# Performance work log

Measured on AMD Instinct MI355X. Metric: run time of the kernel, lower is better.

Reference implementation:

```python
import jax, jax.numpy as jnp
import numpy as np

B, N = 8, 48
NEMBED, EMBED_DIM, HID_DIM = 1000, 32, 32
IN_DIM = EMBED_DIM + 1  # feature dim after concatenating xfeat
N_OPS = 8  # exchangeable 3-tensor basis: identity + means over each nonempty axis subset


def setup_inputs() -> dict:
    key = jax.random.key(0)
    k1, k2, k3, k4, k5 = jax.random.split(key, 5)
    xcat = jax.random.randint(k1, (B, N), 0, NEMBED)
    xfeat = jax.random.normal(k2, (B, N), dtype=jnp.float32)
    embed_table = jax.random.normal(k3, (NEMBED, EMBED_DIM), dtype=jnp.float32)
    # SetEq3to3 coefficients: (in_dim, n_basis_ops, out_dim), Glorot-ish scale
    coefs = jax.random.normal(k4, (IN_DIM, N_OPS, HID_DIM), dtype=jnp.float32) * np.sqrt(2.0 / (IN_DIM + HID_DIM))
    eq_bias = jnp.zeros((HID_DIM,), dtype=jnp.float32)
    out_w = jax.random.normal(k5, (HID_DIM, 1), dtype=jnp.float32) * np.sqrt(1.0 / HID_DIM)
    out_b = jnp.zeros((1,), dtype=jnp.float32)
    return {"xcat": xcat, "xfeat": xfeat, "embed_table": embed_table,
            "coefs": coefs, "eq_bias": eq_bias, "out_w": out_w, "out_b": out_b}


def _set_eq3to3(t, coefs, eq_bias):
    # t: (B, d, n, n, n); coefs: (d, 8, h). Each basis op is a mean over a
    # subset of the three set axes (kept as size-1 dims so broadcasting restores shape).
    def mix(op, s):
        return jnp.einsum('bd...,dh->bh...', op, coefs[:, s, :])
    m_i = t.mean(axis=2, keepdims=True)
    m_j = t.mean(axis=3, keepdims=True)
    m_k = t.mean(axis=4, keepdims=True)
    m_ij = m_i.mean(axis=3, keepdims=True)
    m_ik = m_i.mean(axis=4, keepdims=True)
    m_jk = m_j.mean(axis=4, keepdims=True)
    m_ijk = m_ij.mean(axis=4, keepdims=True)
    out = (mix(t, 0) + mix(m_i, 1) + mix(m_j, 2) + mix(m_k, 3)
           + mix(m_ij, 4) + mix(m_ik, 5) + mix(m_jk, 6) + mix(m_ijk, 7))
    return out + eq_bias.reshape(1, -1, 1, 1, 1)  # (B, h, n, n, n)


def reference(xcat, xfeat, embed_table, coefs, eq_bias, out_w, out_b):
    e = embed_table[xcat]                                   # (B, n, d_e)
    x = jnp.concatenate([e, xfeat[..., None]], axis=-1)      # (B, n, d) with d = d_e + 1
    t = jnp.einsum('bid,bjd,bkd->bdijk', x, x, x)            # (B, d, n, n, n)
    y = _set_eq3to3(t, coefs, eq_bias)                       # (B, h, n, n, n)
    y = jnp.transpose(y, (0, 2, 3, 4, 1))                    # (B, n, n, n, h)
    y = jax.nn.relu(y)
    y = y.mean(axis=(1, 2, 3))                               # (B, h) mean pool
    y = jax.nn.relu(y)
    # dropout is inactive in eval mode (training=False)
    return y @ out_w + out_b                                 # (B, 1)
```

## Files before the change

kernel.cpp:

```cpp
#include <hip/hip_runtime.h>
#include <cstdint>
#include <cstddef>

#define BB 8
#define NN 48
#define DD 33
#define XS 40
#define KP 128
#define HH 32
#define MM (NN*NN)
#define NC (NN*HH)
#define TILE 96
#define TM (MM/TILE)
#define TN (NC/TILE)
#define NBLK (TM*TN)
#define LDK 136
#define ABLK (BB*MM/16)
#define BBLK (BB*NC/16)

typedef __attribute__((ext_vector_type(8))) _Float16 f16x8;
typedef __attribute__((ext_vector_type(4))) float f32x4;

__global__ void k_setup(const int* __restrict__ xcat, const float* __restrict__ xfeat,
                        const float* __restrict__ embed, const float* __restrict__ coefs,
                        const float* __restrict__ eq_bias,
                        float* __restrict__ xw, float* __restrict__ sw,
                        float* __restrict__ ct, float* __restrict__ gk) {
    int b = blockIdx.x, t = threadIdx.x;
    __shared__ float sl[XS];
    if (b < BB) {
        for (int idx = t; idx < NN * XS; idx += 256) {
            int i = idx / XS, d = idx - i * XS;
            float v = 0.f;
            if (d < 32)       v = embed[xcat[b * NN + i] * 32 + d];
            else if (d == 32) v = xfeat[b * NN + i];
            xw[b * NN * XS + idx] = v;
        }
        __syncthreads();
        if (t < XS) {
            float a = 0.f;
            for (int i = 0; i < NN; ++i) a += xw[b * NN * XS + i * XS + t];
            float s = a * (1.0f / 48.0f);
            sw[b * XS + t] = s;
            sl[t] = s;
        }
        __syncthreads();
        for (int idx = t; idx < NC; idx += 256) {
            int k = idx >> 5, h = idx & 31;
            const float* xk = xw + (b * NN + k) * XS;
            float g = 0.f;
            for (int d = 0; d < DD; ++d) {
                float sd = sl[d];
                g += sd * sd * (coefs[(d * 8 + 4) * HH + h] * xk[d]
                              + coefs[(d * 8 + 7) * HH + h] * sd);
            }
            gk[b * NC + idx] = g + eq_bias[h];
        }
    } else {
        for (int idx = t; idx < 8 * HH * XS; idx += 256) {
            int qh = idx / XS, d = idx - qh * XS;
            int q = qh >> 5, h = qh & 31;
            ct[idx] = (d < DD) ? coefs[(d * 8 + q) * HH + h] : 0.f;
        }
    }
}

__global__ __launch_bounds__(256) void k_build(
        const float* __restrict__ xw, const float* __restrict__ sw,
        const float* __restrict__ ct, const float* __restrict__ gk,
        _Float16* __restrict__ Aw, _Float16* __restrict__ Bw) {
    int t = threadIdx.x, blk = blockIdx.x;
    if (blk < ABLK) {
        int g = blk * 256 + t;
        int row = g >> 4, d0 = (g & 15) * 8;
        int b = row / MM, grow = row - b * MM;
        int i = grow / NN, j = grow - i * NN;
        const float* xb = xw + b * NN * XS;
        const float* sb = sw + b * XS;
        f16x8 v;
        if (d0 < 120) {
            int seg = (d0 >= 80) ? 2 : (d0 >= 40) ? 1 : 0;
            int d = d0 - seg * 40;
            const float* p1 = (seg == 2) ? (xb + j * XS) : (xb + i * XS);
            const float* p2 = (seg == 0) ? (xb + j * XS) : sb;
            f32x4 a0 = *(const f32x4*)(p1 + d), a1 = *(const f32x4*)(p1 + d + 4);
            f32x4 b0 = *(const f32x4*)(p2 + d), b1 = *(const f32x4*)(p2 + d + 4);
            f32x4 r0 = a0 * b0, r1 = a1 * b1;
            for (int e = 0; e < 4; ++e) { v[e] = (_Float16)r0[e]; v[4 + e] = (_Float16)r1[e]; }
        } else {
            v = (f16x8){0, 0, 0, 0, 0, 0, 0, 0};
            v[0] = (_Float16)1.f;
        }
        *(f16x8*)&Aw[(size_t)row * KP + d0] = v;
    } else {
        int g = (blk - ABLK) * 256 + t;
        int row = g >> 4, d0 = (g & 15) * 8;
        int b = row / NC, n = row - b * NC;
        int k = n >> 5, h = n & 31;
        const float* xk = xw + (b * NN + k) * XS;
        const float* sb = sw + b * XS;
        f16x8 v;
        if (d0 < 120) {
            int seg = (d0 >= 80) ? 2 : (d0 >= 40) ? 1 : 0;
            int d = d0 - seg * 40;
            const int QA[3] = {0, 2, 1}, QB[3] = {3, 6, 5};
            const float* ca = ct + (QA[seg] * HH + h) * XS + d;
            const float* cb = ct + (QB[seg] * HH + h) * XS + d;
            f32x4 ca0 = *(const f32x4*)(ca),     ca1 = *(const f32x4*)(ca + 4);
            f32x4 cb0 = *(const f32x4*)(cb),     cb1 = *(const f32x4*)(cb + 4);
            f32x4 xk0 = *(const f32x4*)(xk + d), xk1 = *(const f32x4*)(xk + d + 4);
            f32x4 sb0 = *(const f32x4*)(sb + d), sb1 = *(const f32x4*)(sb + d + 4);
            f32x4 r0 = ca0 * xk0 + cb0 * sb0;
            f32x4 r1 = ca1 * xk1 + cb1 * sb1;
            for (int e = 0; e < 4; ++e) { v[e] = (_Float16)r0[e]; v[4 + e] = (_Float16)r1[e]; }
        } else {
            v = (f16x8){0, 0, 0, 0, 0, 0, 0, 0};
            v[0] = (_Float16)gk[b * NC + n];
        }
        *(f16x8*)&Bw[(size_t)row * KP + d0] = v;
    }
}

__global__ __launch_bounds__(256, 3) void k_gemm(
        const _Float16* __restrict__ Aw, const _Float16* __restrict__ Bw,
        float* __restrict__ partials) {
    __shared__ __align__(16) _Float16 As[TILE][LDK];
    __shared__ __align__(16) _Float16 Bs[TILE][LDK];
    __shared__ float hacc[HH];

    int t = threadIdx.x;
    int bx = blockIdx.x, by = blockIdx.y, b = blockIdx.z;
    int N0 = bx * TILE, M0 = by * TILE;
    const _Float16* Ag = Aw + ((size_t)(b * MM + M0)) * KP;
    const _Float16* Bg = Bw + ((size_t)(b * NC + N0)) * KP;

    if (t < HH) hacc[t] = 0.f;

#pragma unroll
    for (int c = 0; c < 6; ++c) {
        int ch = c * 256 + t;
        int row = ch >> 4, d0 = (ch & 15) * 8;
        f16x8 va = *(const f16x8*)(Ag + row * KP + d0);
        f16x8 vb = *(const f16x8*)(Bg + row * KP + d0);
        *(f16x8*)&As[row][d0] = va;
        *(f16x8*)&Bs[row][d0] = vb;
    }
    __syncthreads();

    int lane = t & 63, wave = t >> 6;
    int wm = (wave >> 1) * 48, wn = (wave & 1) * 48;
    int lrow = lane & 15, quad = lane >> 4;

    f32x4 acc[3][3];
#pragma unroll
    for (int m3 = 0; m3 < 3; ++m3)
#pragma unroll
        for (int nt = 0; nt < 3; ++nt)
            acc[m3][nt] = (f32x4){0.f, 0.f, 0.f, 0.f};

#pragma unroll
    for (int ks = 0; ks < 4; ++ks) {
        f16x8 af[3], bf[3];
#pragma unroll
        for (int m3 = 0; m3 < 3; ++m3)
            af[m3] = *(const f16x8*)&As[wm + m3 * 16 + lrow][ks * 32 + quad * 8];
#pragma unroll
        for (int nt = 0; nt < 3; ++nt)
            bf[nt] = *(const f16x8*)&Bs[wn + nt * 16 + lrow][ks * 32 + quad * 8];
#pragma unroll
        for (int m3 = 0; m3 < 3; ++m3)
#pragma unroll
            for (int nt = 0; nt < 3; ++nt)
                acc[m3][nt] = __builtin_amdgcn_mfma_f32_16x16x32_f16(af[m3], bf[nt], acc[m3][nt], 0, 0, 0);
    }

    float fs[3] = {0.f, 0.f, 0.f};
#pragma unroll
    for (int m3 = 0; m3 < 3; ++m3)
#pragma unroll
        for (int nt = 0; nt < 3; ++nt)
#pragma unroll
            for (int r = 0; r < 4; ++r)
                fs[nt] += fmaxf(acc[m3][nt][r], 0.f);

#pragma unroll
    for (int nt = 0; nt < 3; ++nt) {
        float v = fs[nt];
        v += __shfl_xor(v, 16);
        v += __shfl_xor(v, 32);
        if (lane < 16) atomicAdd(&hacc[(wn + nt * 16 + lane) & 31], v);
    }
    __syncthreads();
    if (t < HH) {
        int blockLin = by * TN + bx;
        partials[((size_t)b * NBLK + blockLin) * HH + t] = hacc[t];
    }
}

__global__ void k_final(const float* __restrict__ partials, const float* __restrict__ out_w,
                        const float* __restrict__ out_b, float* __restrict__ out) {
    __shared__ float red[256];
    int b = blockIdx.x, t = threadIdx.x;
    int h = t & 31, g = t >> 5;
    float a = 0.f;
    for (int p = g; p < NBLK; p += 8) a += partials[((size_t)b * NBLK + p) * HH + h];
    red[t] = a;
    __syncthreads();
    if (t < HH) {
        float tot = 0.f;
        for (int gg = 0; gg < 8; ++gg) tot += red[gg * 32 + t];
        float m = tot * (1.0f / 110592.0f);
        red[t] = fmaxf(m, 0.f) * out_w[t];
    }
    __syncthreads();
    if (t == 0) {
        float o = 0.f;
        for (int h2 = 0; h2 < HH; ++h2) o += red[h2];
        out[b] = o + out_b[0];
    }
}

extern "C" void kernel_launch(void* const* d_in, const int* in_sizes, int n_in,
                              void* d_out, int out_size, void* d_ws, size_t ws_size,
                              hipStream_t stream) {
    (void)in_sizes; (void)n_in; (void)out_size; (void)ws_size;
    const int*   xcat    = (const int*)d_in[0];
    const float* xfeat   = (const float*)d_in[1];
    const float* embed   = (const float*)d_in[2];
    const float* coefs   = (const float*)d_in[3];
    const float* eq_bias = (const float*)d_in[4];
    const float* out_w   = (const float*)d_in[5];
    const float* out_b   = (const float*)d_in[6];
    float* out = (float*)d_out;

    char* w = (char*)d_ws;
    float*    xw       = (float*)(w + 0);
    float*    sw       = (float*)(w + 61440);
    float*    ct       = (float*)(w + 62720);
    float*    gk       = (float*)(w + 103680);
    _Float16* Aw       = (_Float16*)(w + 152832);
    _Float16* Bw       = (_Float16*)(w + 4871424);
    float*    partials = (float*)(w + 8017152);

    k_setup<<<dim3(BB + 1), dim3(256), 0, stream>>>(xcat, xfeat, embed, coefs, eq_bias,
                                                    xw, sw, ct, gk);
    k_build<<<dim3(ABLK + BBLK), dim3(256), 0, stream>>>(xw, sw, ct, gk, Aw, Bw);
    k_gemm<<<dim3(TN, TM, BB), dim3(256), 0, stream>>>(Aw, Bw, partials);
    k_final<<<dim3(BB), dim3(256), 0, stream>>>(partials, out_w, out_b, out);
}
```

Measured before the change: 108.7 us.

## Use direct global-to-LDS loads with XOR swizzle in GEMM tile staging

The GEMM kernel now stages its A and B tiles with global_load_lds direct-to-LDS 16-byte loads instead of going through registers. The padded shared layout is replaced by an unpadded one with an XOR swizzle on the source addresses, so the later fragment reads avoid bank conflicts. The setup kernel also caches the embedded rows and two coefficient slices in shared memory instead of rereading global memory. This relies on the per-wave contiguous LDS destination semantics of the builtin and on matching the swizzle between the write and read sides.

```diff
diff --git a/kernel.cpp b/kernel.cpp
--- a/kernel.cpp
+++ b/kernel.cpp
@@ -14,12 +14,17 @@
 #define TM (MM/TILE)
 #define TN (NC/TILE)
 #define NBLK (TM*TN)
-#define LDK 136
 #define ABLK (BB*MM/16)
 #define BBLK (BB*NC/16)
 
 typedef __attribute__((ext_vector_type(8))) _Float16 f16x8;
 typedef __attribute__((ext_vector_type(4))) float f32x4;
+
+__device__ __forceinline__ void gload16(const void* g, void* l) {
+    __builtin_amdgcn_global_load_lds(
+        (const __attribute__((address_space(1))) unsigned int*)g,
+        (__attribute__((address_space(3))) unsigned int*)l, 16, 0, 0);
+}
 
 __global__ void k_setup(const int* __restrict__ xcat, const float* __restrict__ xfeat,
                         const float* __restrict__ embed, const float* __restrict__ coefs,
@@ -27,19 +32,27 @@
                         float* __restrict__ xw, float* __restrict__ sw,
                         float* __restrict__ ct, float* __restrict__ gk) {
     int b = blockIdx.x, t = threadIdx.x;
-    __shared__ float sl[XS];
     if (b < BB) {
+        __shared__ float xl[NN * XS];
+        __shared__ float sl[XS];
+        __shared__ float c47[2][DD][HH];
+        for (int idx = t; idx < 2 * DD * HH; idx += 256) {
+            int q = idx / (DD * HH), r = idx - q * DD * HH;
+            int d = r >> 5, h = r & 31;
+            c47[q][d][h] = coefs[(d * 8 + (q ? 7 : 4)) * HH + h];
+        }
         for (int idx = t; idx < NN * XS; idx += 256) {
             int i = idx / XS, d = idx - i * XS;
             float v = 0.f;
             if (d < 32)       v = embed[xcat[b * NN + i] * 32 + d];
             else if (d == 32) v = xfeat[b * NN + i];
+            xl[idx] = v;
             xw[b * NN * XS + idx] = v;
         }
         __syncthreads();
         if (t < XS) {
             float a = 0.f;
-            for (int i = 0; i < NN; ++i) a += xw[b * NN * XS + i * XS + t];
+            for (int i = 0; i < NN; ++i) a += xl[i * XS + t];
             float s = a * (1.0f / 48.0f);
             sw[b * XS + t] = s;
             sl[t] = s;
@@ -47,12 +60,10 @@
         __syncthreads();
         for (int idx = t; idx < NC; idx += 256) {
             int k = idx >> 5, h = idx & 31;
-            const float* xk = xw + (b * NN + k) * XS;
             float g = 0.f;
             for (int d = 0; d < DD; ++d) {
                 float sd = sl[d];
-                g += sd * sd * (coefs[(d * 8 + 4) * HH + h] * xk[d]
-                              + coefs[(d * 8 + 7) * HH + h] * sd);
+                g += sd * sd * (c47[0][d][h] * xl[k * XS + d] + c47[1][d][h] * sd);
             }
             gk[b * NC + idx] = g + eq_bias[h];
         }
@@ -124,31 +135,29 @@
 __global__ __launch_bounds__(256, 3) void k_gemm(
         const _Float16* __restrict__ Aw, const _Float16* __restrict__ Bw,
         float* __restrict__ partials) {
-    __shared__ __align__(16) _Float16 As[TILE][LDK];
-    __shared__ __align__(16) _Float16 Bs[TILE][LDK];
+    __shared__ __align__(16) _Float16 AsF[TILE * KP];
+    __shared__ __align__(16) _Float16 BsF[TILE * KP];
     __shared__ float hacc[HH];
 
     int t = threadIdx.x;
+    int lane = t & 63, wave = t >> 6;
     int bx = blockIdx.x, by = blockIdx.y, b = blockIdx.z;
     int N0 = bx * TILE, M0 = by * TILE;
-    const _Float16* Ag = Aw + ((size_t)(b * MM + M0)) * KP;
-    const _Float16* Bg = Bw + ((size_t)(b * NC + N0)) * KP;
+    const char* Agc = (const char*)(Aw + ((size_t)(b * MM + M0)) * KP);
+    const char* Bgc = (const char*)(Bw + ((size_t)(b * NC + N0)) * KP);
 
     if (t < HH) hacc[t] = 0.f;
 
 #pragma unroll
     for (int c = 0; c < 6; ++c) {
-        int ch = c * 256 + t;
-        int row = ch >> 4, d0 = (ch & 15) * 8;
-        f16x8 va = *(const f16x8*)(Ag + row * KP + d0);
-        f16x8 vb = *(const f16x8*)(Bg + row * KP + d0);
-        *(f16x8*)&As[row][d0] = va;
-        *(f16x8*)&Bs[row][d0] = vb;
-    }
-    __syncthreads();
-
-    int lane = t & 63, wave = t >> 6;
-    int wm = (wave >> 1) * 48, wn = (wave & 1) * 48;
+        int row0 = c * 16 + wave * 4;
+        int row = row0 + (lane >> 4);
+        int src = row * 256 + (((lane & 15) * 16) ^ ((row & 7) << 4));
+        gload16(Agc + src, (char*)AsF + row0 * 256);
+        gload16(Bgc + src, (char*)BsF + row0 * 256);
+    }
+    __syncthreads();
+
     int lrow = lane & 15, quad = lane >> 4;
 
     f32x4 acc[3][3];
@@ -158,15 +167,21 @@
         for (int nt = 0; nt < 3; ++nt)
             acc[m3][nt] = (f32x4){0.f, 0.f, 0.f, 0.f};
 
+    int wm = (wave >> 1) * 48, wn = (wave & 1) * 48;
 #pragma unroll
     for (int ks = 0; ks < 4; ++ks) {
+        int cb = ks * 64 + quad * 16;
         f16x8 af[3], bf[3];
 #pragma unroll
-        for (int m3 = 0; m3 < 3; ++m3)
-            af[m3] = *(const f16x8*)&As[wm + m3 * 16 + lrow][ks * 32 + quad * 8];
-#pragma unroll
-        for (int nt = 0; nt < 3; ++nt)
-            bf[nt] = *(const f16x8*)&Bs[wn + nt * 16 + lrow][ks * 32 + quad * 8];
+        for (int m3 = 0; m3 < 3; ++m3) {
+            int R = wm + m3 * 16 + lrow;
+            af[m3] = *(const f16x8*)((const char*)AsF + R * 256 + (cb ^ ((R & 7) << 4)));
+        }
+#pragma unroll
+        for (int nt = 0; nt < 3; ++nt) {
+            int R = wn + nt * 16 + lrow;
+            bf[nt] = *(const f16x8*)((const char*)BsF + R * 256 + (cb ^ ((R & 7) << 4)));
+        }
 #pragma unroll
         for (int m3 = 0; m3 < 3; ++m3)
 #pragma unroll
```

Result: no change. 110.4 us (+1.6%).
